# Performance work log

Measured on AMD Instinct MI355X. Metric: run time of the kernel, lower is better.

The kernel has to match this reference:

```python
import jax, jax.numpy as jnp
import numpy as np

MATRIX_SIZE = 64  # m; chol params T = m*(m+1)//2 = 2080
INPUT_SIZE = 512
BATCH = 8192


def setup_inputs() -> dict:
    key = jax.random.key(0)
    k1, k2, k3 = jax.random.split(key, 3)
    T = MATRIX_SIZE * (MATRIX_SIZE + 1) // 2
    x = jax.random.normal(k1, (BATCH, INPUT_SIZE), dtype=jnp.float32)
    # nn.Linear params: W [T, input_size], b [T]
    W = jax.random.normal(k2, (T, INPUT_SIZE), dtype=jnp.float32) / np.sqrt(INPUT_SIZE)
    b = jax.random.normal(k3, (T,), dtype=jnp.float32) * 0.01
    return {"x": x, "W": W, "b": b}


def reference(x, W, b):
    m = MATRIX_SIZE
    # fc: [B, T] Cholesky parameters
    chol = x @ W.T + b
    # Row-major lower-triangle ordering (i, j<=i) matches the original idx loop
    rows, cols = np.tril_indices(m)           # each [T]
    diag = jnp.asarray(rows == cols)           # [T] bool
    # ReLU on diagonal entries, identity off-diagonal (single fused where)
    vals = jnp.where(diag[None, :], jax.nn.relu(chol), chol)  # [B, T]
    B = x.shape[0]
    L = jnp.zeros((B, m, m), dtype=chol.dtype).at[:, rows, cols].set(vals)
    # L @ L^T per batch element -> positive semidefinite [B, m, m]
    return jnp.einsum('bij,bkj->bik', L, L)
```

## Files before the change

### kernel.cpp

```cpp
#include <hip/hip_runtime.h>
#include <stdint.h>

#define MDIM 8192
#define KDIM 512
#define TDIM 2080
#define NPAD 2176
#define MSZ  64

typedef __attribute__((ext_vector_type(8))) __bf16 bf16x8;
typedef __attribute__((ext_vector_type(4))) float  f32x4;

__device__ __forceinline__ unsigned short f2bf(float f) {
    unsigned int u = __float_as_uint(f);
    u += 0x7fffu + ((u >> 16) & 1u);
    return (unsigned short)(u >> 16);
}

__device__ __forceinline__ int tril_row(int n) {
    int i = (int)((sqrtf((float)(8 * n + 1)) - 1.0f) * 0.5f);
    while ((i + 1) * (i + 2) / 2 <= n) ++i;
    while (i * (i + 1) / 2 > n) --i;
    return i;
}

#define NX4 (MDIM * KDIM / 4)
#define NW4 (NPAD * KDIM / 4)
#define NT4 (NPAD / 4)

__global__ __launch_bounds__(256) void convert_kernel(const float* __restrict__ x,
                                                      const float* __restrict__ W,
                                                      const float* __restrict__ b,
                                                      unsigned short* __restrict__ xb,
                                                      unsigned short* __restrict__ wb,
                                                      float* __restrict__ biasf,
                                                      float* __restrict__ diagm) {
    int idx = blockIdx.x * 256 + threadIdx.x;
    if (idx < NX4) {
        float4 v = reinterpret_cast<const float4*>(x)[idx];
        reinterpret_cast<ushort4*>(xb)[idx] =
            make_ushort4(f2bf(v.x), f2bf(v.y), f2bf(v.z), f2bf(v.w));
    } else if (idx < NX4 + NW4) {
        int j = idx - NX4;
        int n = (j * 4) >> 9;
        ushort4 o = make_ushort4(0, 0, 0, 0);
        if (n < TDIM) {
            float4 v = reinterpret_cast<const float4*>(W)[j];
            o = make_ushort4(f2bf(v.x), f2bf(v.y), f2bf(v.z), f2bf(v.w));
        }
        reinterpret_cast<ushort4*>(wb)[j] = o;
    } else {
        int t = idx - NX4 - NW4;
        if (t < NT4) {
#pragma unroll
            for (int r = 0; r < 4; ++r) {
                int n = t * 4 + r;
                float bv = 0.f, dm = 0.f;
                if (n < TDIM) {
                    bv = b[n];
                    int i = tril_row(n);
                    dm = (n - i * (i + 1) / 2 == i) ? 1.f : 0.f;
                }
                biasf[n] = bv;
                diagm[n] = dm;
            }
        }
    }
}

typedef __attribute__((address_space(1))) void as1_void;
typedef __attribute__((address_space(3))) void as3_void;

__device__ __forceinline__ void gload_lds16(const void* g, void* l) {
    __builtin_amdgcn_global_load_lds((as1_void*)(void*)g, (as3_void*)l, 16, 0, 0);
}

__device__ __forceinline__ bf16x8 frag_load(const unsigned short* base, int row, int kbyte) {
    kbyte ^= (row & 7) << 4;
    return *reinterpret_cast<const bf16x8*>(reinterpret_cast<const char*>(base) + row * 128 + kbyte);
}

__global__ __launch_bounds__(256) void gemm_kernel(const unsigned short* __restrict__ xb,
                                                   const unsigned short* __restrict__ wb,
                                                   const float* __restrict__ biasf,
                                                   const float* __restrict__ diagm,
                                                   unsigned short* __restrict__ chol) {
    __shared__ __align__(16) unsigned short As[128 * 64];
    __shared__ __align__(16) unsigned short Bs[128 * 64];
    const int tid  = threadIdx.x;
    const int lane = tid & 63;
    const int wave = tid >> 6;

    const int bid = blockIdx.x;
    const int xcd = bid & 7;
    const int c   = bid >> 3;
    const int mt  = xcd * 8 + c / 17;
    const int nt  = c % 17;
    const int m0 = mt * 128;
    const int n0 = nt * 128;

    const int wm = (wave >> 1) * 64;
    const int wn = (wave & 1) * 64;
    const int lr = lane & 15;
    const int lq = lane >> 4;

    f32x4 acc[4][4];
    f32x4 zero = {0.f, 0.f, 0.f, 0.f};
#pragma unroll
    for (int i = 0; i < 4; ++i)
#pragma unroll
        for (int j = 0; j < 4; ++j) acc[i][j] = zero;

    for (int k0 = 0; k0 < KDIM; k0 += 64) {
        const unsigned short* ga = xb + (size_t)m0 * KDIM + k0;
        const unsigned short* gb = wb + (size_t)n0 * KDIM + k0;
#pragma unroll
        for (int cc = 0; cc < 4; ++cc) {
            int flat = cc * 256 + tid;
            int row  = flat >> 3;
            int ch   = (flat & 7) ^ (row & 7);
            unsigned short* lb = (unsigned short*)As + (size_t)(cc * 256 + (tid & 192)) * 8;
            gload_lds16(ga + row * KDIM + ch * 8, lb);
        }
#pragma unroll
        for (int cc = 0; cc < 4; ++cc) {
            int flat = cc * 256 + tid;
            int row  = flat >> 3;
            int ch   = (flat & 7) ^ (row & 7);
            unsigned short* lb = (unsigned short*)Bs + (size_t)(cc * 256 + (tid & 192)) * 8;
            gload_lds16(gb + row * KDIM + ch * 8, lb);
        }
        __syncthreads();
#pragma unroll
        for (int kk = 0; kk < 2; ++kk) {
            bf16x8 af[4], bf[4];
            int kb = kk * 64 + lq * 16;
#pragma unroll
            for (int i = 0; i < 4; ++i) {
                af[i] = frag_load(As, wm + i * 16 + lr, kb);
                bf[i] = frag_load(Bs, wn + i * 16 + lr, kb);
            }
#pragma unroll
            for (int mi = 0; mi < 4; ++mi)
#pragma unroll
                for (int ni = 0; ni < 4; ++ni)
                    acc[mi][ni] = __builtin_amdgcn_mfma_f32_16x16x32_bf16(bf[ni], af[mi], acc[mi][ni], 0, 0, 0);
        }
        __syncthreads();
    }

    const float4* bt = reinterpret_cast<const float4*>(biasf);
    const float4* dt = reinterpret_cast<const float4*>(diagm);
#pragma unroll
    for (int ni = 0; ni < 4; ++ni) {
        int nb = n0 + wn + ni * 16 + lq * 4;
        float4 bv = bt[nb >> 2];
        float4 dm = dt[nb >> 2];
#pragma unroll
        for (int mi = 0; mi < 4; ++mi) {
            int m = m0 + wm + mi * 16 + lr;
            float v0 = acc[mi][ni][0] + bv.x; if (dm.x != 0.f && v0 < 0.f) v0 = 0.f;
            float v1 = acc[mi][ni][1] + bv.y; if (dm.y != 0.f && v1 < 0.f) v1 = 0.f;
            float v2 = acc[mi][ni][2] + bv.z; if (dm.z != 0.f && v2 < 0.f) v2 = 0.f;
            float v3 = acc[mi][ni][3] + bv.w; if (dm.w != 0.f && v3 < 0.f) v3 = 0.f;
            *reinterpret_cast<ushort4*>(&chol[(size_t)m * NPAD + nb]) =
                make_ushort4(f2bf(v0), f2bf(v1), f2bf(v2), f2bf(v3));
        }
    }
}

__device__ __forceinline__ void lds_store_swz(unsigned short* L, int i, int j, unsigned short v) {
    int ch   = ((j >> 3) ^ i) & 7;
    int addr = i * 128 + (ch << 4) + ((j & 7) * 2);
    *reinterpret_cast<unsigned short*>(reinterpret_cast<char*>(L) + addr) = v;
}

__global__ __launch_bounds__(256) void syrk_kernel(const unsigned short* __restrict__ chol,
                                                   float* __restrict__ out) {
    __shared__ __align__(16) unsigned short Ls[4][64 * 64];
    const int tid  = threadIdx.x;
    const int lane = tid & 63;
    const int wave = tid >> 6;

    const int bid = blockIdx.x;
    const int bb  = (bid & 7) * 256 + (bid >> 3);
    const int batch = bb * 4 + wave;
    unsigned short* L = Ls[wave];

    const unsigned int* row = reinterpret_cast<const unsigned int*>(chol + (size_t)batch * NPAD);
    unsigned int vals[17];
#pragma unroll
    for (int c = 0; c < 17; ++c) {
        int t = lane + c * 64;
        vals[c] = (t < TDIM / 2) ? row[t] : 0u;
    }

#pragma unroll
    for (int c = 0; c < 8; ++c)
        *reinterpret_cast<int4*>(reinterpret_cast<char*>(L) + (c * 64 + lane) * 16) = make_int4(0, 0, 0, 0);
    __builtin_amdgcn_sched_barrier(0);

#pragma unroll
    for (int c = 0; c < 17; ++c) {
        int t = lane + c * 64;
        if (t < TDIM / 2) {
            unsigned int v = vals[c];
            int n = 2 * t;
            int i = tril_row(n);
            int j = n - i * (i + 1) / 2;
            lds_store_swz(L, i, j, (unsigned short)(v & 0xffffu));
            int i2 = i, j2 = j + 1;
            if (j2 > i2) { i2 = i + 1; j2 = 0; }
            lds_store_swz(L, i2, j2, (unsigned short)(v >> 16));
        }
    }
    asm volatile("s_waitcnt lgkmcnt(0)" ::: "memory");
    __builtin_amdgcn_sched_barrier(0);

    const int lr = lane & 15;
    const int lq = lane >> 4;
    bf16x8 fr[4][2];
#pragma unroll
    for (int i = 0; i < 4; ++i)
#pragma unroll
        for (int kk = 0; kk < 2; ++kk)
            fr[i][kk] = frag_load(L, i * 16 + lr, kk * 64 + lq * 16);

    f32x4 acc[4][4];
    f32x4 zero = {0.f, 0.f, 0.f, 0.f};
#pragma unroll
    for (int i = 0; i < 4; ++i)
#pragma unroll
        for (int j = 0; j < 4; ++j) acc[i][j] = zero;

#pragma unroll
    for (int mi = 0; mi < 4; ++mi)
#pragma unroll
        for (int ni = 0; ni < 4; ++ni)
#pragma unroll
            for (int kk = 0; kk < 2; ++kk)
                acc[mi][ni] = __builtin_amdgcn_mfma_f32_16x16x32_bf16(fr[mi][kk], fr[ni][kk], acc[mi][ni], 0, 0, 0);

    float* ob = out + (size_t)batch * (MSZ * MSZ);
#pragma unroll
    for (int mi = 0; mi < 4; ++mi)
#pragma unroll
        for (int ni = 0; ni < 4; ++ni)
            *reinterpret_cast<f32x4*>(ob + (ni * 16 + lr) * MSZ + mi * 16 + lq * 4) = acc[mi][ni];
}

extern "C" void kernel_launch(void* const* d_in, const int* in_sizes, int n_in,
                              void* d_out, int out_size, void* d_ws, size_t ws_size,
                              hipStream_t stream) {
    (void)in_sizes; (void)n_in; (void)out_size; (void)ws_size;
    const float* x = (const float*)d_in[0];
    const float* W = (const float*)d_in[1];
    const float* b = (const float*)d_in[2];
    float* out = (float*)d_out;

    unsigned short* xb   = (unsigned short*)d_ws;
    unsigned short* wb   = xb + (size_t)MDIM * KDIM;
    unsigned short* chol = wb + (size_t)NPAD * KDIM;
    float* biasf = (float*)(chol + (size_t)MDIM * NPAD);
    float* diagm = biasf + NPAD;

    int conv_blocks = (NX4 + NW4 + NT4 + 255) / 256;
    convert_kernel<<<dim3(conv_blocks), dim3(256), 0, stream>>>(x, W, b, xb, wb, biasf, diagm);
    gemm_kernel<<<dim3(17 * 64), dim3(256), 0, stream>>>(xb, wb, biasf, diagm, chol);
    syrk_kernel<<<dim3(MDIM / 4), dim3(256), 0, stream>>>(chol, out);
}
```

Before: 74.05 us.

## Rewrite GEMM as 8-wave 256x128 tile with triple-buffered LDS pipeline

The GEMM stage now uses 512-thread blocks computing 256x128 tiles, with a three-deep LDS ring buffer fed by direct global-to-LDS loads issued two k-steps ahead. Loads are interleaved with fragment reads, each MFMA cluster is raised to high priority with s_setprio, and explicit vmcnt waits and barriers order the stages. The goal is to hide global load latency behind MFMA work and improve reuse per block. The cost is more LDS (144 KB) and one block per CU, with correctness depending on the hand-placed waitcnt and barrier logic.

```diff
diff --git a/kernel.cpp b/kernel.cpp
--- a/kernel.cpp
+++ b/kernel.cpp
@@ -6,6 +6,12 @@
 #define TDIM 2080
 #define NPAD 2176
 #define MSZ  64
+
+#define BM 256
+#define BN 128
+#define BK 64
+#define BUF_ELEMS 24576
+#define BOFF      16384
 
 typedef __attribute__((ext_vector_type(8))) __bf16 bf16x8;
 typedef __attribute__((ext_vector_type(4))) float  f32x4;
@@ -79,13 +85,12 @@
     return *reinterpret_cast<const bf16x8*>(reinterpret_cast<const char*>(base) + row * 128 + kbyte);
 }
 
-__global__ __launch_bounds__(256) void gemm_kernel(const unsigned short* __restrict__ xb,
-                                                   const unsigned short* __restrict__ wb,
-                                                   const float* __restrict__ biasf,
-                                                   const float* __restrict__ diagm,
-                                                   unsigned short* __restrict__ chol) {
-    __shared__ __align__(16) unsigned short As[128 * 64];
-    __shared__ __align__(16) unsigned short Bs[128 * 64];
+__global__ __launch_bounds__(512, 1) void gemm8_kernel(const unsigned short* __restrict__ xb,
+                                                       const unsigned short* __restrict__ wb,
+                                                       const float* __restrict__ biasf,
+                                                       const float* __restrict__ diagm,
+                                                       unsigned short* __restrict__ chol) {
+    __shared__ __align__(16) unsigned short S[3 * BUF_ELEMS];
     const int tid  = threadIdx.x;
     const int lane = tid & 63;
     const int wave = tid >> 6;
@@ -93,16 +98,38 @@
     const int bid = blockIdx.x;
     const int xcd = bid & 7;
     const int c   = bid >> 3;
-    const int mt  = xcd * 8 + c / 17;
+    const int mt  = xcd * 4 + c / 17;
     const int nt  = c % 17;
-    const int m0 = mt * 128;
-    const int n0 = nt * 128;
-
-    const int wm = (wave >> 1) * 64;
-    const int wn = (wave & 1) * 64;
+    const int m0 = mt * BM;
+    const int n0 = nt * BN;
+
+    const int wr = wave >> 1;
+    const int wc = wave & 1;
+    const int wm = wr * 64;
+    const int wn = wc * 64;
     const int lr = lane & 15;
     const int lq = lane >> 4;
 
+    const int rS = tid >> 3;
+    const unsigned short* gA = xb + (size_t)m0 * KDIM;
+    const unsigned short* gB = wb + (size_t)n0 * KDIM;
+    const int waveOff = (tid & 448) * 8;
+
+#define STAGE_A(KT, A)                                                              \
+    {                                                                               \
+        int row = (A) * 64 + rS;                                                    \
+        int ch  = (tid & 7) ^ (row & 7);                                            \
+        gload_lds16(gA + (size_t)row * KDIM + (KT) * BK + ch * 8,                   \
+                    &S[((KT) % 3) * BUF_ELEMS + (A) * 4096 + waveOff]);             \
+    }
+#define STAGE_B(KT, B)                                                              \
+    {                                                                               \
+        int row = (B) * 64 + rS;                                                    \
+        int ch  = (tid & 7) ^ (row & 7);                                            \
+        gload_lds16(gB + (size_t)row * KDIM + (KT) * BK + ch * 8,                   \
+                    &S[((KT) % 3) * BUF_ELEMS + BOFF + (B) * 4096 + waveOff]);      \
+    }
+
     f32x4 acc[4][4];
     f32x4 zero = {0.f, 0.f, 0.f, 0.f};
 #pragma unroll
@@ -110,43 +137,56 @@
 #pragma unroll
         for (int j = 0; j < 4; ++j) acc[i][j] = zero;
 
-    for (int k0 = 0; k0 < KDIM; k0 += 64) {
-        const unsigned short* ga = xb + (size_t)m0 * KDIM + k0;
-        const unsigned short* gb = wb + (size_t)n0 * KDIM + k0;
-#pragma unroll
-        for (int cc = 0; cc < 4; ++cc) {
-            int flat = cc * 256 + tid;
-            int row  = flat >> 3;
-            int ch   = (flat & 7) ^ (row & 7);
-            unsigned short* lb = (unsigned short*)As + (size_t)(cc * 256 + (tid & 192)) * 8;
-            gload_lds16(ga + row * KDIM + ch * 8, lb);
-        }
-#pragma unroll
-        for (int cc = 0; cc < 4; ++cc) {
-            int flat = cc * 256 + tid;
-            int row  = flat >> 3;
-            int ch   = (flat & 7) ^ (row & 7);
-            unsigned short* lb = (unsigned short*)Bs + (size_t)(cc * 256 + (tid & 192)) * 8;
-            gload_lds16(gb + row * KDIM + ch * 8, lb);
-        }
-        __syncthreads();
-#pragma unroll
-        for (int kk = 0; kk < 2; ++kk) {
-            bf16x8 af[4], bf[4];
-            int kb = kk * 64 + lq * 16;
-#pragma unroll
-            for (int i = 0; i < 4; ++i) {
-                af[i] = frag_load(As, wm + i * 16 + lr, kb);
-                bf[i] = frag_load(Bs, wn + i * 16 + lr, kb);
+    STAGE_A(0, 0) STAGE_A(0, 1) STAGE_A(0, 2) STAGE_A(0, 3) STAGE_B(0, 0) STAGE_B(0, 1)
+    STAGE_A(1, 0) STAGE_A(1, 1) STAGE_A(1, 2) STAGE_A(1, 3) STAGE_B(1, 0) STAGE_B(1, 1)
+    asm volatile("s_waitcnt vmcnt(6)" ::: "memory");
+    __builtin_amdgcn_s_barrier();
+
+#pragma unroll
+    for (int kt = 0; kt < 8; ++kt) {
+        const unsigned short* Ab = &S[(kt % 3) * BUF_ELEMS];
+        const unsigned short* Bb = Ab + BOFF;
+#pragma unroll
+        for (int p = 0; p < 4; ++p) {
+            const int mq = (p >> 1) * 2;
+            const int nq = (p & 1) * 2;
+            bf16x8 a00 = frag_load(Ab, wm + (mq + 0) * 16 + lr, 0 * 64 + lq * 16);
+            bf16x8 a01 = frag_load(Ab, wm + (mq + 0) * 16 + lr, 1 * 64 + lq * 16);
+            bf16x8 a10 = frag_load(Ab, wm + (mq + 1) * 16 + lr, 0 * 64 + lq * 16);
+            bf16x8 a11 = frag_load(Ab, wm + (mq + 1) * 16 + lr, 1 * 64 + lq * 16);
+            bf16x8 b00 = frag_load(Bb, wn + (nq + 0) * 16 + lr, 0 * 64 + lq * 16);
+            bf16x8 b01 = frag_load(Bb, wn + (nq + 0) * 16 + lr, 1 * 64 + lq * 16);
+            bf16x8 b10 = frag_load(Bb, wn + (nq + 1) * 16 + lr, 0 * 64 + lq * 16);
+            bf16x8 b11 = frag_load(Bb, wn + (nq + 1) * 16 + lr, 1 * 64 + lq * 16);
+            if (kt < 6) {
+                if (p == 0)      { STAGE_A(kt + 2, 0) STAGE_A(kt + 2, 1) }
+                else if (p == 1) { STAGE_A(kt + 2, 2) STAGE_A(kt + 2, 3) }
+                else if (p == 2) { STAGE_B(kt + 2, 0) }
+                else             { STAGE_B(kt + 2, 1) }
             }
-#pragma unroll
-            for (int mi = 0; mi < 4; ++mi)
-#pragma unroll
-                for (int ni = 0; ni < 4; ++ni)
-                    acc[mi][ni] = __builtin_amdgcn_mfma_f32_16x16x32_bf16(bf[ni], af[mi], acc[mi][ni], 0, 0, 0);
-        }
-        __syncthreads();
-    }
+            __builtin_amdgcn_s_barrier();
+            asm volatile("s_waitcnt lgkmcnt(0)" ::: "memory");
+            __builtin_amdgcn_sched_barrier(0);
+            __builtin_amdgcn_s_setprio(1);
+            acc[mq + 0][nq + 0] = __builtin_amdgcn_mfma_f32_16x16x32_bf16(b00, a00, acc[mq + 0][nq + 0], 0, 0, 0);
+            acc[mq + 0][nq + 0] = __builtin_amdgcn_mfma_f32_16x16x32_bf16(b01, a01, acc[mq + 0][nq + 0], 0, 0, 0);
+            acc[mq + 0][nq + 1] = __builtin_amdgcn_mfma_f32_16x16x32_bf16(b10, a00, acc[mq + 0][nq + 1], 0, 0, 0);
+            acc[mq + 0][nq + 1] = __builtin_amdgcn_mfma_f32_16x16x32_bf16(b11, a01, acc[mq + 0][nq + 1], 0, 0, 0);
+            acc[mq + 1][nq + 0] = __builtin_amdgcn_mfma_f32_16x16x32_bf16(b00, a10, acc[mq + 1][nq + 0], 0, 0, 0);
+            acc[mq + 1][nq + 0] = __builtin_amdgcn_mfma_f32_16x16x32_bf16(b01, a11, acc[mq + 1][nq + 0], 0, 0, 0);
+            acc[mq + 1][nq + 1] = __builtin_amdgcn_mfma_f32_16x16x32_bf16(b10, a10, acc[mq + 1][nq + 1], 0, 0, 0);
+            acc[mq + 1][nq + 1] = __builtin_amdgcn_mfma_f32_16x16x32_bf16(b11, a11, acc[mq + 1][nq + 1], 0, 0, 0);
+            __builtin_amdgcn_s_setprio(0);
+            __builtin_amdgcn_sched_barrier(0);
+            if (p == 3) {
+                if (kt < 6)       { asm volatile("s_waitcnt vmcnt(6)" ::: "memory"); }
+                else if (kt == 6) { asm volatile("s_waitcnt vmcnt(0)" ::: "memory"); }
+            }
+            __builtin_amdgcn_s_barrier();
+        }
+    }
+#undef STAGE_A
+#undef STAGE_B
 
     const float4* bt = reinterpret_cast<const float4*>(biasf);
     const float4* dt = reinterpret_cast<const float4*>(diagm);
@@ -265,6 +305,6 @@
 
     int conv_blocks = (NX4 + NW4 + NT4 + 255) / 256;
     convert_kernel<<<dim3(conv_blocks), dim3(256), 0, stream>>>(x, W, b, xb, wb, biasf, diagm);
-    gemm_kernel<<<dim3(17 * 64), dim3(256), 0, stream>>>(xb, wb, biasf, diagm, chol);
+    gemm8_kernel<<<dim3(544), dim3(512), 0, stream>>>(xb, wb, biasf, diagm, chol);
     syrk_kernel<<<dim3(MDIM / 4), dim3(256), 0, stream>>>(chol, out);
 }
```

Result: slower. 85.26 us (+15.1%).
